# Performance work log

Hardware: AMD Instinct MI355X
Metric: run time of the kernel (lower is better)

## Reference

```python
import jax, jax.numpy as jnp
import numpy as np

B, C, N = 8, 128, 4096
C2 = C // 2
BN_EPS = 1e-5


def setup_inputs() -> dict:
    key = jax.random.key(0)
    ks = jax.random.split(key, 8)
    s = 1.0 / np.sqrt(C)
    s2 = 1.0 / np.sqrt(C2)
    return {
        "x": jax.random.normal(ks[0], (B, C, N), dtype=jnp.float32),
        "w_qk": jax.random.uniform(ks[1], (C2, C), jnp.float32, -s, s),  # shared q/k weight
        "w_v": jax.random.uniform(ks[2], (C2, C), jnp.float32, -s, s),
        "b_v": jax.random.uniform(ks[3], (C2,), jnp.float32, -s, s),
        "w_x": jax.random.uniform(ks[4], (C2, C), jnp.float32, -s, s),
        "w_t": jax.random.uniform(ks[5], (C2, C2), jnp.float32, -s2, s2),
        "b_t": jax.random.uniform(ks[6], (C2,), jnp.float32, -s2, s2),
        "gamma": jnp.ones((C2,), jnp.float32),
        "beta": jnp.zeros((C2,), jnp.float32),
    }


def reference(x, w_qk, w_v, b_v, w_x, w_t, b_t, gamma, beta):
    # 1x1 convs are per-point linear maps: [B,C,N] -> [B,C2,N]
    x_q = jnp.einsum("oc,bcn->bno", w_qk, x)          # [B, N, C2]
    x_k = jnp.einsum("oc,bcn->bon", w_qk, x)          # [B, C2, N]
    x_v = jnp.einsum("oc,bcn->bon", w_v, x) + b_v[None, :, None]

    energy = jnp.einsum("bno,bom->bnm", x_q, x_k)     # [B, N, N]
    attn = jax.nn.softmax(energy, axis=-1)            # row softmax
    attn = attn / (1e-9 + attn.sum(axis=1, keepdims=True))  # column L1 renorm

    x_r = jnp.einsum("bon,bnm->bom", x_v, attn)       # [B, C2, N]
    x_c = jnp.einsum("oc,bcn->bon", w_x, x)           # [B, C2, N]

    d = x_c - x_r
    t = jnp.einsum("oi,bin->bon", w_t, d) + b_t[None, :, None]
    # BatchNorm1d (training-mode batch stats) over (B, N) per channel
    mean = t.mean(axis=(0, 2), keepdims=True)
    var = t.var(axis=(0, 2), keepdims=True)
    t_hat = (t - mean) * jax.lax.rsqrt(var + BN_EPS)
    x_r2 = jax.nn.relu(gamma[None, :, None] * t_hat + beta[None, :, None])
    return x_c + x_r2
```

## Files before the change

kernel.cpp:

```cpp
#include <hip/hip_runtime.h>

#define B_   8
#define C_   128
#define N_   4096
#define C2_  64

typedef __bf16 bf16x8 __attribute__((ext_vector_type(8)));
typedef float  f32x4  __attribute__((ext_vector_type(4)));

#define MFMA16(a, b, c) __builtin_amdgcn_mfma_f32_16x16x32_bf16((a), (b), (c), 0, 0, 0)

#define QK_SCALE 1.2011224087864498f

static __device__ __forceinline__ unsigned short f2bf(float f) {
    union { __bf16 b; unsigned short u; } cv;
    cv.b = (__bf16)f;
    return cv.u;
}

struct us4 { unsigned short a, b, c, d; };

static __device__ __forceinline__ void gl_lds16(const unsigned short* g, void* l) {
    __builtin_amdgcn_global_load_lds(
        (const __attribute__((address_space(1))) unsigned int*)g,
        (__attribute__((address_space(3))) unsigned int*)l,
        16, 0, 0);
}

__global__ __launch_bounds__(256) void k1_proj(
    const float* __restrict__ x, const float* __restrict__ w_qk,
    const float* __restrict__ w_v, const float* __restrict__ b_v,
    const float* __restrict__ w_x,
    unsigned short* __restrict__ qk_t, unsigned short* __restrict__ xv_bf,
    float* __restrict__ xc)
{
    __shared__ __align__(16) unsigned short w_lds[192 * 136];
    __shared__ __align__(16) unsigned short x_t[64 * 136];
    const int tid = threadIdx.x;
    const int wave = tid >> 6, lane = tid & 63;
    const int quad = lane >> 4, col = lane & 15;
    const int b = blockIdx.y;
    const int n0 = blockIdx.x * 64;

    const float* wsrc[3] = {w_qk, w_v, w_x};
    #pragma unroll
    for (int mat = 0; mat < 3; ++mat) {
        const float* wm = wsrc[mat];
        #pragma unroll
        for (int it = 0; it < 8; ++it) {
            const int idx = it * 256 + tid;
            const int o = idx >> 5, c = (idx & 31) * 4;
            const float4 v = *(const float4*)(wm + o * C_ + c);
            us4 pk;
            pk.a = f2bf(v.x); pk.b = f2bf(v.y); pk.c = f2bf(v.z); pk.d = f2bf(v.w);
            *(us4*)&w_lds[(mat * 64 + o) * 136 + c] = pk;
        }
    }
    const float* xb = x + (size_t)b * C_ * N_ + n0;
    #pragma unroll
    for (int it = 0; it < 8; ++it) {
        const int idx = it * 256 + tid;
        const int c = idx >> 4, n = (idx & 15) * 4;
        const float4 v = *(const float4*)(xb + (size_t)c * N_ + n);
        x_t[(n + 0) * 136 + c] = f2bf(v.x);
        x_t[(n + 1) * 136 + c] = f2bf(v.y);
        x_t[(n + 2) * 136 + c] = f2bf(v.z);
        x_t[(n + 3) * 136 + c] = f2bf(v.w);
    }
    __syncthreads();

    const int nw = wave * 16;
    bf16x8 bfr[4];
    #pragma unroll
    for (int kt = 0; kt < 4; ++kt)
        bfr[kt] = *(const bf16x8*)&x_t[(nw + col) * 136 + kt * 32 + quad * 8];

    const int n_g = n0 + nw + col;

    #pragma unroll
    for (int ot = 0; ot < 12; ++ot) {
        f32x4 acc = {0.f, 0.f, 0.f, 0.f};
        #pragma unroll
        for (int kt = 0; kt < 4; ++kt) {
            const bf16x8 afr = *(const bf16x8*)&w_lds[(ot * 16 + col) * 136 + kt * 32 + quad * 8];
            acc = MFMA16(afr, bfr[kt], acc);
        }
        if (ot < 4) {
            us4 pk;
            pk.a = f2bf(acc[0] * QK_SCALE); pk.b = f2bf(acc[1] * QK_SCALE);
            pk.c = f2bf(acc[2] * QK_SCALE); pk.d = f2bf(acc[3] * QK_SCALE);
            *(us4*)&qk_t[(size_t)(b * N_ + n_g) * C2_ + ot * 16 + quad * 4] = pk;
        } else if (ot < 8) {
            const float4 bv4 = *(const float4*)(b_v + (ot - 4) * 16 + quad * 4);
            const float* bvp = (const float*)&bv4;
            #pragma unroll
            for (int r = 0; r < 4; ++r)
                xv_bf[(size_t)(b * C2_ + (ot - 4) * 16 + quad * 4 + r) * N_ + n_g]
                    = f2bf(acc[r] + bvp[r]);
        } else {
            #pragma unroll
            for (int r = 0; r < 4; ++r)
                xc[(size_t)(b * C2_ + (ot - 8) * 16 + quad * 4 + r) * N_ + n_g] = acc[r];
        }
    }
}

__global__ __launch_bounds__(256) void k2_rowstats(
    const unsigned short* __restrict__ qk_t, float* __restrict__ part_rs)
{
    __shared__ __align__(16) unsigned char lds_raw[2 * 8192];
    const int tid = threadIdx.x;
    const int wave = tid >> 6, lane = tid & 63;
    const int quad = lane >> 4, col = lane & 15;
    const int b = blockIdx.x & 7;
    const int nblk = (blockIdx.x >> 3) & 63;
    const int mq = blockIdx.x >> 9;
    const int n_base = nblk * 64 + wave * 16;
    const int m_start = mq * 1024;
    const unsigned short* qb = qk_t + (size_t)b * N_ * C2_;

    const bf16x8 a0 = *(const bf16x8*)(qb + (size_t)(n_base + col) * C2_ + quad * 8);
    const bf16x8 a1 = *(const bf16x8*)(qb + (size_t)(n_base + col) * C2_ + quad * 8 + 32);

    auto stage = [&](int m0, int p) {
        unsigned char* base = lds_raw + p * 8192;
        #pragma unroll
        for (int r = 0; r < 2; ++r) {
            const int idx = r * 256 + tid;
            const int row = idx >> 3, seg = idx & 7;
            gl_lds16(qb + (size_t)(m0 + row) * C2_ + (size_t)(seg ^ (row & 7)) * 8,
                     base + idx * 16);
        }
    };

    float run_s[4] = {0.f, 0.f, 0.f, 0.f};
    stage(m_start, 0);
    __syncthreads();

    for (int c = 0; c < 16; ++c) {
        const int p = c & 1;
        if (c + 1 < 16) stage(m_start + (c + 1) * 64, 1 - p);
        const unsigned short* qt = (const unsigned short*)(lds_raw + p * 8192);
        #pragma unroll
        for (int ms = 0; ms < 4; ++ms) {
            const int row = ms * 16 + col;
            const bf16x8 b0 = *(const bf16x8*)(qt + row * 64 + ((quad ^ (col & 7)) * 8));
            const bf16x8 b1 = *(const bf16x8*)(qt + row * 64 + (((4 + quad) ^ (col & 7)) * 8));
            f32x4 acc = {0.f, 0.f, 0.f, 0.f};
            acc = MFMA16(a0, b0, acc);
            acc = MFMA16(a1, b1, acc);
            #pragma unroll
            for (int r = 0; r < 4; ++r)
                run_s[r] += __builtin_amdgcn_exp2f(acc[r]);
        }
        __syncthreads();
    }

    #pragma unroll
    for (int r = 0; r < 4; ++r) {
        #pragma unroll
        for (int off = 1; off < 16; off <<= 1)
            run_s[r] += __shfl_xor(run_s[r], off, 64);
    }
    if (col == 0) {
        #pragma unroll
        for (int r = 0; r < 4; ++r)
            part_rs[((size_t)(mq * 8 + b) << 12) + n_base + quad * 4 + r] = run_s[r];
    }
}

__global__ __launch_bounds__(256) void k2b_comb(
    const float* __restrict__ part_rs, float* __restrict__ rowoff)
{
    const int i = blockIdx.x * 256 + threadIdx.x;
    const int b = i >> 12, n = i & 4095;
    float s = 0.f;
    #pragma unroll
    for (int q = 0; q < 4; ++q)
        s += part_rs[((size_t)(q * 8 + b) << 12) + n];
    rowoff[i] = __builtin_amdgcn_logf(s);
}

__global__ __launch_bounds__(256) void k3_pv(
    const unsigned short* __restrict__ qk_t, const unsigned short* __restrict__ xv_bf,
    const float* __restrict__ rowoff, float* __restrict__ yp0, float* __restrict__ yp1,
    float* __restrict__ cspart)
{
    __shared__ __align__(16) unsigned char lds_raw[32768 + 8 * 2304];
    const int tid = threadIdx.x;
    const int wave = tid >> 6, lane = tid & 63;
    const int quad = lane >> 4, col = lane & 15;
    const int b = blockIdx.x & 7;
    const int m_blk = ((blockIdx.x >> 3) & 31) * 128;
    const int nh = blockIdx.x >> 8;
    const int n_start = nh * 2048;
    const int m_wave = m_blk + wave * 32;
    const unsigned short* qb = qk_t + (size_t)b * N_ * C2_;
    const unsigned short* vb = xv_bf + (size_t)b * C2_ * N_;
    const float* ro = rowoff + b * N_;
    float* yp = nh ? yp1 : yp0;

    bf16x8 kb0[2], kb1[2];
    #pragma unroll
    for (int g = 0; g < 2; ++g) {
        const unsigned short* p = qb + (size_t)(m_wave + g * 16 + col) * C2_ + quad * 8;
        kb0[g] = *(const bf16x8*)p;
        kb1[g] = *(const bf16x8*)(p + 32);
    }

    unsigned short (*st_s[2])[72];
    st_s[0] = (unsigned short(*)[72])(lds_raw + 32768 + (wave * 2 + 0) * 2304);
    st_s[1] = (unsigned short(*)[72])(lds_raw + 32768 + (wave * 2 + 1) * 2304);

    auto stage = [&](int n0, int p) {
        unsigned char* qbase = lds_raw + p * 8192;
        unsigned char* vbase = lds_raw + 16384 + p * 8192;
        #pragma unroll
        for (int r = 0; r < 2; ++r) {
            const int idx = r * 256 + tid;
            const int row = idx >> 3, seg = idx & 7;
            const int ss = seg ^ (row & 7);
            gl_lds16(qb + (size_t)(n0 + row) * C2_ + (size_t)ss * 8, qbase + idx * 16);
            gl_lds16(vb + (size_t)row * N_ + n0 + ss * 8, vbase + idx * 16);
        }
    };

    f32x4 accY[2][4];
    #pragma unroll
    for (int g = 0; g < 2; ++g)
        #pragma unroll
        for (int os = 0; os < 4; ++os) accY[g][os] = (f32x4){0.f, 0.f, 0.f, 0.f};
    float colacc[2] = {0.f, 0.f};

    stage(n_start, 0);
    __syncthreads();

    for (int c = 0; c < 32; ++c) {
        const int n0 = n_start + c * 64;
        const int p = c & 1;
        if (c + 1 < 32) stage(n0 + 64, 1 - p);

        float4 ro4[4];
        #pragma unroll
        for (int ns = 0; ns < 4; ++ns)
            ro4[ns] = *(const float4*)(ro + n0 + ns * 16 + quad * 4);

        const unsigned short* qt = (const unsigned short*)(lds_raw + p * 8192);
        const unsigned short* vt = (const unsigned short*)(lds_raw + 16384 + p * 8192);

        #pragma unroll
        for (int ns = 0; ns < 4; ++ns) {
            const int row = ns * 16 + col;
            const bf16x8 qa0 = *(const bf16x8*)(qt + row * 64 + ((quad ^ (col & 7)) * 8));
            const bf16x8 qa1 = *(const bf16x8*)(qt + row * 64 + (((4 + quad) ^ (col & 7)) * 8));
            const float* rr = (const float*)&ro4[ns];
            #pragma unroll
            for (int g = 0; g < 2; ++g) {
                f32x4 acc = {0.f, 0.f, 0.f, 0.f};
                acc = MFMA16(qa0, kb0[g], acc);
                acc = MFMA16(qa1, kb1[g], acc);
                union { unsigned short us[4]; uint2 u2; } pk;
                #pragma unroll
                for (int r = 0; r < 4; ++r) {
                    const float s = __builtin_amdgcn_exp2f(acc[r] - rr[r]);
                    colacc[g] += s;
                    pk.us[r] = f2bf(s);
                }
                *(uint2*)&st_s[g][col][ns * 16 + quad * 4] = pk.u2;
            }
        }

        bf16x8 sB0[2], sB1[2];
        #pragma unroll
        for (int g = 0; g < 2; ++g) {
            sB0[g] = *(const bf16x8*)&st_s[g][col][quad * 8];
            sB1[g] = *(const bf16x8*)&st_s[g][col][32 + quad * 8];
        }
        #pragma unroll
        for (int os = 0; os < 4; ++os) {
            const int o = os * 16 + col;
            const bf16x8 va0 = *(const bf16x8*)(vt + o * 64 + ((quad ^ (col & 7)) * 8));
            const bf16x8 va1 = *(const bf16x8*)(vt + o * 64 + (((4 + quad) ^ (col & 7)) * 8));
            #pragma unroll
            for (int g = 0; g < 2; ++g) {
                accY[g][os] = MFMA16(va0, sB0[g], accY[g][os]);
                accY[g][os] = MFMA16(va1, sB1[g], accY[g][os]);
            }
        }
        __syncthreads();
    }

    #pragma unroll
    for (int g = 0; g < 2; ++g) {
        colacc[g] += __shfl_xor(colacc[g], 16, 64);
        colacc[g] += __shfl_xor(colacc[g], 32, 64);
        if (lane < 16)
            cspart[((size_t)nh * 8 + b) * N_ + m_wave + g * 16 + col] = colacc[g];
        #pragma unroll
        for (int os = 0; os < 4; ++os)
            #pragma unroll
            for (int r = 0; r < 4; ++r)
                yp[(size_t)(b * C2_ + os * 16 + quad * 4 + r) * N_ + m_wave + g * 16 + col]
                    = accY[g][os][r];
    }
}

__global__ __launch_bounds__(256) void k3b_comb(
    float* yp0, const float* __restrict__ yp1,
    const float* __restrict__ cspart)
{
    const int idx4 = blockIdx.x * 256 + threadIdx.x;
    const int b = idx4 >> 16;
    const int m4 = idx4 & 1023;
    const float4 y0 = ((const float4*)yp0)[idx4];
    const float4 y1 = ((const float4*)yp1)[idx4];
    const float4 c0 = ((const float4*)cspart)[b * 1024 + m4];
    const float4 c1 = ((const float4*)cspart)[8192 + b * 1024 + m4];
    float4 r;
    r.x = (y0.x + y1.x) / (1e-9f + c0.x + c1.x);
    r.y = (y0.y + y1.y) / (1e-9f + c0.y + c1.y);
    r.z = (y0.z + y1.z) / (1e-9f + c0.z + c1.z);
    r.w = (y0.w + y1.w) / (1e-9f + c0.w + c1.w);
    ((float4*)yp0)[idx4] = r;
}

__global__ __launch_bounds__(256) void k4_t(
    const float* __restrict__ xc, const float* __restrict__ xr,
    const float* __restrict__ w_t, const float* __restrict__ b_t,
    float* __restrict__ t_buf)
{
    __shared__ float d_lds[64][64];
    __shared__ float w_lds[64][64];
    const int b = blockIdx.y;
    const int n0 = blockIdx.x * 64;
    const size_t base = (size_t)b * C2_ * N_;

    for (int idx = threadIdx.x; idx < 4096; idx += 256) {
        const int i = idx >> 6, n = idx & 63;
        const size_t g = base + (size_t)i * N_ + n0 + n;
        d_lds[i][n] = xc[g] - xr[g];
        w_lds[i][n] = w_t[idx];
    }
    __syncthreads();

    const int n = threadIdx.x & 63, ow = (threadIdx.x >> 6) * 16;
    float acc[16];
    #pragma unroll
    for (int oo = 0; oo < 16; ++oo) acc[oo] = 0.f;
    for (int i = 0; i < 64; ++i) {
        const float dv = d_lds[i][n];
        #pragma unroll
        for (int oo = 0; oo < 16; ++oo)
            acc[oo] += w_lds[ow + oo][i] * dv;
    }
    #pragma unroll
    for (int oo = 0; oo < 16; ++oo)
        t_buf[base + (size_t)(ow + oo) * N_ + n0 + n] = acc[oo] + b_t[ow + oo];
}

__global__ __launch_bounds__(256) void k5_bnstats(
    const float* __restrict__ t_buf, float* __restrict__ bn)
{
    const int o = blockIdx.x;
    float s = 0.f, s2 = 0.f;
    for (int b = 0; b < B_; ++b) {
        const float4* p = (const float4*)(t_buf + (size_t)(b * C2_ + o) * N_);
        for (int j = threadIdx.x; j < N_ / 4; j += 256) {
            const float4 v = p[j];
            s  += v.x + v.y + v.z + v.w;
            s2 += v.x * v.x + v.y * v.y + v.z * v.z + v.w * v.w;
        }
    }
    #pragma unroll
    for (int off = 1; off < 64; off <<= 1) {
        s  += __shfl_xor(s, off, 64);
        s2 += __shfl_xor(s2, off, 64);
    }
    __shared__ float red[2][4];
    if ((threadIdx.x & 63) == 0) {
        red[0][threadIdx.x >> 6] = s;
        red[1][threadIdx.x >> 6] = s2;
    }
    __syncthreads();
    if (threadIdx.x == 0) {
        bn[o]       = red[0][0] + red[0][1] + red[0][2] + red[0][3];
        bn[64 + o]  = red[1][0] + red[1][1] + red[1][2] + red[1][3];
    }
}

__global__ __launch_bounds__(256) void k6_out(
    const float* __restrict__ xc, const float* __restrict__ t_buf,
    const float* __restrict__ bn, const float* __restrict__ gamma,
    const float* __restrict__ beta, float* __restrict__ out)
{
    const int idx = blockIdx.x * 256 + threadIdx.x;
    const int o = (idx >> 10) & 63;
    const float invC = 1.0f / (float)(B_ * N_);
    const float mean = bn[o] * invC;
    const float var  = bn[64 + o] * invC - mean * mean;
    const float sc = gamma[o] * rsqrtf(var + 1e-5f);
    const float sh = beta[o] - mean * sc;
    const float4 t4 = ((const float4*)t_buf)[idx];
    const float4 c4 = ((const float4*)xc)[idx];
    float4 r;
    r.x = c4.x + fmaxf(0.f, sc * t4.x + sh);
    r.y = c4.y + fmaxf(0.f, sc * t4.y + sh);
    r.z = c4.z + fmaxf(0.f, sc * t4.z + sh);
    r.w = c4.w + fmaxf(0.f, sc * t4.w + sh);
    ((float4*)out)[idx] = r;
}

extern "C" void kernel_launch(void* const* d_in, const int* in_sizes, int n_in,
                              void* d_out, int out_size, void* d_ws, size_t ws_size,
                              hipStream_t stream) {
    const float* x     = (const float*)d_in[0];
    const float* w_qk  = (const float*)d_in[1];
    const float* w_v   = (const float*)d_in[2];
    const float* b_v   = (const float*)d_in[3];
    const float* w_x   = (const float*)d_in[4];
    const float* w_t   = (const float*)d_in[5];
    const float* b_t   = (const float*)d_in[6];
    const float* gamma = (const float*)d_in[7];
    const float* beta  = (const float*)d_in[8];
    float* out = (float*)d_out;

    char* ws = (char*)d_ws;
    unsigned short* qk_t  = (unsigned short*)ws;
    unsigned short* xv_bf = (unsigned short*)(ws + (4  << 20));
    float* xc      = (float*)(ws + (8  << 20));
    float* xr_yp0  = (float*)(ws + (16 << 20));
    float* tb_yp1  = (float*)(ws + (24 << 20));
    float* part_rs = (float*)(ws + (32 << 20));
    float* rowoff  = (float*)(ws + (32 << 20) + (512 << 10));
    float* cspart  = (float*)(ws + (32 << 20) + (640 << 10));
    float* bn      = (float*)(ws + (32 << 20) + (896 << 10));

    hipLaunchKernelGGL(k1_proj,     dim3(64, 8),  256, 0, stream,
                       x, w_qk, w_v, b_v, w_x, qk_t, xv_bf, xc);
    hipLaunchKernelGGL(k2_rowstats, dim3(2048),   256, 0, stream, qk_t, part_rs);
    hipLaunchKernelGGL(k2b_comb,    dim3(128),    256, 0, stream, part_rs, rowoff);
    hipLaunchKernelGGL(k3_pv,       dim3(512),    256, 0, stream,
                       qk_t, xv_bf, rowoff, xr_yp0, tb_yp1, cspart);
    hipLaunchKernelGGL(k3b_comb,    dim3(2048),   256, 0, stream, xr_yp0, tb_yp1, cspart);
    hipLaunchKernelGGL(k4_t,        dim3(64, 8),  256, 0, stream, xc, xr_yp0, w_t, b_t, tb_yp1);
    hipLaunchKernelGGL(k5_bnstats,  dim3(64),     256, 0, stream, tb_yp1, bn);
    hipLaunchKernelGGL(k6_out,      dim3(2048),   256, 0, stream, xc, tb_yp1, bn, gamma, beta, out);
}
```

Baseline: 201.4 us.

## Split PV kernel three ways over N and double rows per wave in rowstats

The PV kernel now splits the reduction dimension into three uneven chunks (22/21/21 tiles) instead of two. This raises the grid from 512 to 768 blocks to fill more of the CUs, and the combine kernel gains a third partial. The third partial output buffer reuses the final output array as scratch, and cspart grows so the bn buffer moves. Separately, the rowstats kernel has each wave handle 32 rows instead of 16, reusing each LDS B-fragment across two MFMA pairs and halving its grid and LDS traffic per row.

```diff
diff --git a/kernel.cpp b/kernel.cpp
--- a/kernel.cpp
+++ b/kernel.cpp
@@ -113,14 +113,19 @@
     const int wave = tid >> 6, lane = tid & 63;
     const int quad = lane >> 4, col = lane & 15;
     const int b = blockIdx.x & 7;
-    const int nblk = (blockIdx.x >> 3) & 63;
-    const int mq = blockIdx.x >> 9;
-    const int n_base = nblk * 64 + wave * 16;
+    const int nblk = (blockIdx.x >> 3) & 31;
+    const int mq = blockIdx.x >> 8;
+    const int n_base = nblk * 128 + wave * 32;
     const int m_start = mq * 1024;
     const unsigned short* qb = qk_t + (size_t)b * N_ * C2_;
 
-    const bf16x8 a0 = *(const bf16x8*)(qb + (size_t)(n_base + col) * C2_ + quad * 8);
-    const bf16x8 a1 = *(const bf16x8*)(qb + (size_t)(n_base + col) * C2_ + quad * 8 + 32);
+    bf16x8 a0[2], a1[2];
+    #pragma unroll
+    for (int s = 0; s < 2; ++s) {
+        const unsigned short* p = qb + (size_t)(n_base + s * 16 + col) * C2_ + quad * 8;
+        a0[s] = *(const bf16x8*)p;
+        a1[s] = *(const bf16x8*)(p + 32);
+    }
 
     auto stage = [&](int m0, int p) {
         unsigned char* base = lds_raw + p * 8192;
@@ -133,7 +138,7 @@
         }
     };
 
-    float run_s[4] = {0.f, 0.f, 0.f, 0.f};
+    float run_s[2][4] = {{0.f, 0.f, 0.f, 0.f}, {0.f, 0.f, 0.f, 0.f}};
     stage(m_start, 0);
     __syncthreads();
 
@@ -146,26 +151,34 @@
             const int row = ms * 16 + col;
             const bf16x8 b0 = *(const bf16x8*)(qt + row * 64 + ((quad ^ (col & 7)) * 8));
             const bf16x8 b1 = *(const bf16x8*)(qt + row * 64 + (((4 + quad) ^ (col & 7)) * 8));
-            f32x4 acc = {0.f, 0.f, 0.f, 0.f};
-            acc = MFMA16(a0, b0, acc);
-            acc = MFMA16(a1, b1, acc);
+            #pragma unroll
+            for (int s = 0; s < 2; ++s) {
+                f32x4 acc = {0.f, 0.f, 0.f, 0.f};
+                acc = MFMA16(a0[s], b0, acc);
+                acc = MFMA16(a1[s], b1, acc);
+                #pragma unroll
+                for (int r = 0; r < 4; ++r)
+                    run_s[s][r] += __builtin_amdgcn_exp2f(acc[r]);
+            }
+        }
+        __syncthreads();
+    }
+
+    #pragma unroll
+    for (int s = 0; s < 2; ++s)
+        #pragma unroll
+        for (int r = 0; r < 4; ++r) {
+            #pragma unroll
+            for (int off = 1; off < 16; off <<= 1)
+                run_s[s][r] += __shfl_xor(run_s[s][r], off, 64);
+        }
+    if (col == 0) {
+        #pragma unroll
+        for (int s = 0; s < 2; ++s)
             #pragma unroll
             for (int r = 0; r < 4; ++r)
-                run_s[r] += __builtin_amdgcn_exp2f(acc[r]);
-        }
-        __syncthreads();
-    }
-
-    #pragma unroll
-    for (int r = 0; r < 4; ++r) {
-        #pragma unroll
-        for (int off = 1; off < 16; off <<= 1)
-            run_s[r] += __shfl_xor(run_s[r], off, 64);
-    }
-    if (col == 0) {
-        #pragma unroll
-        for (int r = 0; r < 4; ++r)
-            part_rs[((size_t)(mq * 8 + b) << 12) + n_base + quad * 4 + r] = run_s[r];
+                part_rs[((size_t)(mq * 8 + b) << 12) + n_base + s * 16 + quad * 4 + r]
+                    = run_s[s][r];
     }
 }
 
@@ -184,7 +197,7 @@
 __global__ __launch_bounds__(256) void k3_pv(
     const unsigned short* __restrict__ qk_t, const unsigned short* __restrict__ xv_bf,
     const float* __restrict__ rowoff, float* __restrict__ yp0, float* __restrict__ yp1,
-    float* __restrict__ cspart)
+    float* __restrict__ yp2, float* __restrict__ cspart)
 {
     __shared__ __align__(16) unsigned char lds_raw[32768 + 8 * 2304];
     const int tid = threadIdx.x;
@@ -192,13 +205,14 @@
     const int quad = lane >> 4, col = lane & 15;
     const int b = blockIdx.x & 7;
     const int m_blk = ((blockIdx.x >> 3) & 31) * 128;
-    const int nh = blockIdx.x >> 8;
-    const int n_start = nh * 2048;
+    const int sk = blockIdx.x >> 8;
+    const int n_start = (sk == 0) ? 0 : 1408 + (sk - 1) * 1344;
+    const int n_chunks = (sk == 0) ? 22 : 21;
     const int m_wave = m_blk + wave * 32;
     const unsigned short* qb = qk_t + (size_t)b * N_ * C2_;
     const unsigned short* vb = xv_bf + (size_t)b * C2_ * N_;
     const float* ro = rowoff + b * N_;
-    float* yp = nh ? yp1 : yp0;
+    float* yp = (sk == 0) ? yp0 : (sk == 1) ? yp1 : yp2;
 
     bf16x8 kb0[2], kb1[2];
     #pragma unroll
@@ -235,10 +249,10 @@
     stage(n_start, 0);
     __syncthreads();
 
-    for (int c = 0; c < 32; ++c) {
+    for (int c = 0; c < n_chunks; ++c) {
         const int n0 = n_start + c * 64;
         const int p = c & 1;
-        if (c + 1 < 32) stage(n0 + 64, 1 - p);
+        if (c + 1 < n_chunks) stage(n0 + 64, 1 - p);
 
         float4 ro4[4];
         #pragma unroll
@@ -295,7 +309,7 @@
         colacc[g] += __shfl_xor(colacc[g], 16, 64);
         colacc[g] += __shfl_xor(colacc[g], 32, 64);
         if (lane < 16)
-            cspart[((size_t)nh * 8 + b) * N_ + m_wave + g * 16 + col] = colacc[g];
+            cspart[((size_t)sk * 8 + b) * N_ + m_wave + g * 16 + col] = colacc[g];
         #pragma unroll
         for (int os = 0; os < 4; ++os)
             #pragma unroll
@@ -306,7 +320,7 @@
 }
 
 __global__ __launch_bounds__(256) void k3b_comb(
-    float* yp0, const float* __restrict__ yp1,
+    float* yp0, const float* __restrict__ yp1, const float* __restrict__ yp2,
     const float* __restrict__ cspart)
 {
     const int idx4 = blockIdx.x * 256 + threadIdx.x;
@@ -314,13 +328,15 @@
     const int m4 = idx4 & 1023;
     const float4 y0 = ((const float4*)yp0)[idx4];
     const float4 y1 = ((const float4*)yp1)[idx4];
+    const float4 y2 = ((const float4*)yp2)[idx4];
     const float4 c0 = ((const float4*)cspart)[b * 1024 + m4];
     const float4 c1 = ((const float4*)cspart)[8192 + b * 1024 + m4];
+    const float4 c2 = ((const float4*)cspart)[16384 + b * 1024 + m4];
     float4 r;
-    r.x = (y0.x + y1.x) / (1e-9f + c0.x + c1.x);
-    r.y = (y0.y + y1.y) / (1e-9f + c0.y + c1.y);
-    r.z = (y0.z + y1.z) / (1e-9f + c0.z + c1.z);
-    r.w = (y0.w + y1.w) / (1e-9f + c0.w + c1.w);
+    r.x = (y0.x + y1.x + y2.x) / (1e-9f + c0.x + c1.x + c2.x);
+    r.y = (y0.y + y1.y + y2.y) / (1e-9f + c0.y + c1.y + c2.y);
+    r.z = (y0.z + y1.z + y2.z) / (1e-9f + c0.z + c1.z + c2.z);
+    r.w = (y0.w + y1.w + y2.w) / (1e-9f + c0.w + c1.w + c2.w);
     ((float4*)yp0)[idx4] = r;
 }
 
@@ -433,15 +449,16 @@
     float* part_rs = (float*)(ws + (32 << 20));
     float* rowoff  = (float*)(ws + (32 << 20) + (512 << 10));
     float* cspart  = (float*)(ws + (32 << 20) + (640 << 10));
-    float* bn      = (float*)(ws + (32 << 20) + (896 << 10));
+    float* bn      = (float*)(ws + (33 << 20));
+    float* yp2     = out;
 
     hipLaunchKernelGGL(k1_proj,     dim3(64, 8),  256, 0, stream,
                        x, w_qk, w_v, b_v, w_x, qk_t, xv_bf, xc);
-    hipLaunchKernelGGL(k2_rowstats, dim3(2048),   256, 0, stream, qk_t, part_rs);
+    hipLaunchKernelGGL(k2_rowstats, dim3(1024),   256, 0, stream, qk_t, part_rs);
     hipLaunchKernelGGL(k2b_comb,    dim3(128),    256, 0, stream, part_rs, rowoff);
-    hipLaunchKernelGGL(k3_pv,       dim3(512),    256, 0, stream,
-                       qk_t, xv_bf, rowoff, xr_yp0, tb_yp1, cspart);
-    hipLaunchKernelGGL(k3b_comb,    dim3(2048),   256, 0, stream, xr_yp0, tb_yp1, cspart);
+    hipLaunchKernelGGL(k3_pv,       dim3(768),    256, 0, stream,
+                       qk_t, xv_bf, rowoff, xr_yp0, tb_yp1, yp2, cspart);
+    hipLaunchKernelGGL(k3b_comb,    dim3(2048),   256, 0, stream, xr_yp0, tb_yp1, yp2, cspart);
     hipLaunchKernelGGL(k4_t,        dim3(64, 8),  256, 0, stream, xc, xr_yp0, w_t, b_t, tb_yp1);
     hipLaunchKernelGGL(k5_bnstats,  dim3(64),     256, 0, stream, tb_yp1, bn);
     hipLaunchKernelGGL(k6_out,      dim3(2048),   256, 0, stream, xc, tb_yp1, bn, gamma, beta, out);
```

Result: faster. 197.0 us (-2.2%).
